# Kernel tuning notes

Measured on AMD Instinct MI355X. Metric: run time of the kernel, lower is better.

The kernel has to match this reference:

```python
import jax, jax.numpy as jnp
import numpy as np
import math

C, F, NH, W = 8, 256, 8, 1024  # channels, features (h), num_heads, frames (w)


def conv3x3(x, w):
    # x: [b,c,h,w], w: [out_c,in_c,3,3], padding=1, stride=1, no bias
    return jax.lax.conv_general_dilated(
        x, w, window_strides=(1, 1), padding=((1, 1), (1, 1)),
        dimension_numbers=("NCHW", "OIHW", "NCHW"))


def mc_linear_pw(x, w_pw):
    # per-channel linear over the feature (h) axis
    # x: [b,c,h,w], w_pw: [c, h_out, h_in] -> [b,c,h_out,w]
    return jnp.einsum("bchw,cgh->bcgw", x, w_pw)


def setup_inputs() -> dict:
    key = jax.random.key(0)
    ks = jax.random.split(key, 11)
    conv_s = 1.0 / math.sqrt(C * 9)
    pw_s = 1.0 / math.sqrt(F)
    dw_s = 1.0 / math.sqrt(C)
    return {
        "x": jax.random.normal(ks[0], (1, C, F, W), jnp.float32),
        "prev_qk": jax.random.normal(ks[1], (1, C, NH, W, W), jnp.float32),
        "wq_conv": jax.random.normal(ks[2], (C, C, 3, 3), jnp.float32) * conv_s,
        "wk_conv": jax.random.normal(ks[3], (C, C, 3, 3), jnp.float32) * conv_s,
        "wv_conv": jax.random.normal(ks[4], (C, C, 3, 3), jnp.float32) * conv_s,
        "wq_pw": jax.random.normal(ks[5], (C, F, F), jnp.float32) * pw_s,
        "wk_pw": jax.random.normal(ks[6], (C, F, F), jnp.float32) * pw_s,
        "wv_pw": jax.random.normal(ks[7], (C, F, F), jnp.float32) * pw_s,
        "wo_dw": jax.random.normal(ks[8], (C, C), jnp.float32) * dw_s,
        "wo_pw": jax.random.normal(ks[9], (C, F, F), jnp.float32) * pw_s,
    }


def reference(x, prev_qk, wq_conv, wk_conv, wv_conv, wq_pw, wk_pw, wv_pw, wo_dw, wo_pw):
    b, c, h, w = x.shape
    dh = h // NH

    def proj_heads(inp, w_conv, w_pw):
        p = mc_linear_pw(conv3x3(inp, w_conv), w_pw)          # [b,c,h,w]
        p = jnp.transpose(p, (0, 1, 3, 2))                     # [b,c,w,h]
        p = p.reshape(b, c, w, NH, dh)                         # [b,c,w,nh,dh]
        return jnp.transpose(p, (0, 1, 3, 2, 4))               # [b,c,nh,w,dh]

    q = proj_heads(x, wq_conv, wq_pw)
    k = proj_heads(x, wk_conv, wk_pw)
    v = proj_heads(x, wv_conv, wv_pw)

    # attention in fp32 over the frame (w) axis, scaled by sqrt(h) (features)
    qk = jnp.einsum("bcnqd,bcnkd->bcnqk", q.astype(jnp.float32), k.astype(jnp.float32)) / math.sqrt(h)
    qk = qk + prev_qk
    a = jnp.einsum("bcnqk,bcnkd->bcnqd", jax.nn.softmax(qk, axis=-1), v.astype(jnp.float32))
    a = jnp.transpose(a, (0, 1, 3, 2, 4)).reshape(b, c, w, h)  # [b,c,w,h]
    a = jnp.transpose(a, (0, 1, 3, 2))                          # [b,c,h,w]

    # o_proj: depthwise channel mix then per-channel positionwise linear
    o = jnp.einsum("bchw,dc->bdhw", a, wo_dw)
    out = mc_linear_pw(o, wo_pw)
    return (out, qk)
```

## Files before the change

kernel.cpp:

```cpp
#include <hip/hip_runtime.h>
#include <hip/hip_bf16.h>


typedef float f32x4 __attribute__((ext_vector_type(4)));
typedef short s16x8 __attribute__((ext_vector_type(8)));

static __device__ __forceinline__ unsigned short f2bf(float f) {
  unsigned int u = __builtin_bit_cast(unsigned int, f);
  u += 0x7fff + ((u >> 16) & 1);
  return (unsigned short)(u >> 16);
}

__global__ __launch_bounds__(256) void cvt_weights(
    const float* __restrict__ wq, const float* __restrict__ wk,
    const float* __restrict__ wv, const float* __restrict__ wo,
    unsigned short* __restrict__ dst) {
  int gid = blockIdx.x * 256 + threadIdx.x;
  int e = gid * 4;
  int arr = e >> 19;
  int off = e & 524287;
  const float* src = arr == 0 ? wq : arr == 1 ? wk : arr == 2 ? wv : wo;
  float4 v = *(const float4*)(src + off);
  ushort4 o;
  o.x = f2bf(v.x); o.y = f2bf(v.y); o.z = f2bf(v.z); o.w = f2bf(v.w);
  *(ushort4*)(dst + (size_t)arr * 524288 + off) = o;
}

__global__ __launch_bounds__(256) void conv3x3_k(
    const float* __restrict__ x,
    const float* __restrict__ wq, const float* __restrict__ wk,
    const float* __restrict__ wv,
    unsigned short* __restrict__ convT) {
  __shared__ float xt[8][34][36];
  int t = blockIdx.z;
  const float* wc = (t == 0) ? wq : (t == 1) ? wk : wv;
  int wtile = blockIdx.x * 32, htile = blockIdx.y * 32;
  int tid = threadIdx.x;
  for (int i = tid; i < 8 * 34 * 34; i += 256) {
    int cp = i / 1156;
    int rem = i - cp * 1156;
    int hh = rem / 34, ww = rem - hh * 34;
    int gh = htile + hh - 1, gw = wtile + ww - 1;
    float v = 0.f;
    if ((unsigned)gh < 256u && (unsigned)gw < 1024u)
      v = x[((size_t)cp * 256 + gh) * 1024 + gw];
    xt[cp][hh][ww] = v;
  }
  __syncthreads();
  int tx = tid & 31, strip = tid >> 5;
  int h0 = strip * 4;
  float acc[8][4];
#pragma unroll
  for (int co = 0; co < 8; ++co)
#pragma unroll
    for (int p = 0; p < 4; ++p) acc[co][p] = 0.f;
#pragma unroll 1
  for (int cp = 0; cp < 8; ++cp) {
    float xv[6][3];
#pragma unroll
    for (int rr = 0; rr < 6; ++rr)
#pragma unroll
      for (int cc = 0; cc < 3; ++cc)
        xv[rr][cc] = xt[cp][h0 + rr][tx + cc];
#pragma unroll
    for (int i = 0; i < 3; ++i)
#pragma unroll
      for (int j = 0; j < 3; ++j) {
#pragma unroll
        for (int co = 0; co < 8; ++co) {
          float wgt = wc[((co * 8 + cp) * 3 + i) * 3 + j];
#pragma unroll
          for (int p = 0; p < 4; ++p)
            acc[co][p] += wgt * xv[p + i][j];
        }
      }
  }
  int w = wtile + tx;
#pragma unroll
  for (int co = 0; co < 8; ++co) {
    ushort4 o;
    o.x = f2bf(acc[co][0]); o.y = f2bf(acc[co][1]);
    o.z = f2bf(acc[co][2]); o.w = f2bf(acc[co][3]);
    *(ushort4*)(convT + ((size_t)(t * 8 + co) * 1024 + w) * 256 + htile + h0) = o;
  }
}

__global__ __launch_bounds__(256) void gemm_pw(
    const unsigned short* __restrict__ A0,
    const unsigned short* __restrict__ B0,
    unsigned short* __restrict__ qkh,
    unsigned short* __restrict__ vstd,
    float* __restrict__ outp,
    int mode) {
  int b = blockIdx.z;
  const unsigned short* A = A0 + (size_t)b * 65536;
  const unsigned short* B = B0 + (size_t)b * 262144;
  int lane = threadIdx.x & 63, wvid = threadIdx.x >> 6;
  int wm = wvid & 1, wn = wvid >> 1;
  int mBase = blockIdx.y * 128 + wm * 64;
  int nBase = blockIdx.x * 128 + wn * 64;
  int c15 = lane & 15, klo = (lane >> 4) * 8;
  f32x4 acc[4][4];
#pragma unroll
  for (int mi = 0; mi < 4; ++mi)
#pragma unroll
    for (int ni = 0; ni < 4; ++ni) acc[mi][ni] = (f32x4){0.f, 0.f, 0.f, 0.f};
#pragma unroll 2
  for (int kk = 0; kk < 256; kk += 32) {
    s16x8 af[4], bf[4];
#pragma unroll
    for (int mi = 0; mi < 4; ++mi)
      af[mi] = *(const s16x8*)(A + (size_t)(mBase + mi * 16 + c15) * 256 + kk + klo);
#pragma unroll
    for (int ni = 0; ni < 4; ++ni)
      bf[ni] = *(const s16x8*)(B + (size_t)(nBase + ni * 16 + c15) * 256 + kk + klo);
#pragma unroll
    for (int mi = 0; mi < 4; ++mi)
#pragma unroll
      for (int ni = 0; ni < 4; ++ni)
        acc[mi][ni] = __builtin_amdgcn_mfma_f32_16x16x32_bf16(
            af[mi], bf[ni], acc[mi][ni], 0, 0, 0);
  }
  int r0 = (lane >> 4) * 4;
  if (mode == 0) {
    int t = b >> 3, c = b & 7;
    if (t < 2) {
      unsigned short* dst = qkh + (size_t)t * 2097152 + (size_t)c * 262144;
#pragma unroll
      for (int mi = 0; mi < 4; ++mi)
#pragma unroll
        for (int ni = 0; ni < 4; ++ni) {
          int g = mBase + mi * 16 + r0;
          int w = nBase + ni * 16 + c15;
          int n = g >> 5, d = g & 31;
          ushort4 o;
          o.x = f2bf(acc[mi][ni][0]); o.y = f2bf(acc[mi][ni][1]);
          o.z = f2bf(acc[mi][ni][2]); o.w = f2bf(acc[mi][ni][3]);
          *(ushort4*)(dst + ((size_t)n * 1024 + w) * 32 + d) = o;
        }
    } else {
      unsigned short* dst = vstd + (size_t)c * 262144;
#pragma unroll
      for (int mi = 0; mi < 4; ++mi)
#pragma unroll
        for (int ni = 0; ni < 4; ++ni) {
          int w = nBase + ni * 16 + c15;
#pragma unroll
          for (int r = 0; r < 4; ++r)
            dst[(size_t)(mBase + mi * 16 + r0 + r) * 1024 + w] = f2bf(acc[mi][ni][r]);
        }
    }
  } else {
    float* dst = outp + (size_t)b * 262144;
#pragma unroll
    for (int mi = 0; mi < 4; ++mi)
#pragma unroll
      for (int ni = 0; ni < 4; ++ni) {
        int w = nBase + ni * 16 + c15;
#pragma unroll
        for (int r = 0; r < 4; ++r)
          dst[(size_t)(mBase + mi * 16 + r0 + r) * 1024 + w] = acc[mi][ni][r];
      }
  }
}

__global__ __launch_bounds__(256) void attn_k(
    const unsigned short* __restrict__ Qh,
    const unsigned short* __restrict__ Kh,
    const unsigned short* __restrict__ Vstd,
    const float* __restrict__ prev,
    float* __restrict__ qkOut,
    float* __restrict__ aOut) {
  __shared__ unsigned short plds[4][16 * 72];
  int lane = threadIdx.x & 63, wvid = threadIdx.x >> 6;
  int cn = blockIdx.y;
  int c = cn >> 3, n = cn & 7;
  int qBase = blockIdx.x * 64 + wvid * 16;
  int c15 = lane & 15, quad = lane >> 4, klo = quad * 8;
  const unsigned short* Q = Qh + (size_t)cn * 32768;
  const unsigned short* K = Kh + (size_t)cn * 32768;
  const unsigned short* V = Vstd + (size_t)c * 262144 + (size_t)n * 32 * 1024;
  const float* prevB = prev + (size_t)cn * 1048576 + (size_t)(qBase + c15) * 1024 + quad * 4;
  float* qkB = qkOut + (size_t)cn * 1048576 + (size_t)(qBase + c15) * 1024 + quad * 4;
  s16x8 qf = *(const s16x8*)(Q + (size_t)(qBase + c15) * 32 + klo);
  f32x4 o0 = {0.f, 0.f, 0.f, 0.f}, o1 = {0.f, 0.f, 0.f, 0.f};
  float lsum = 0.f;
  unsigned short* pw = plds[wvid];

  f32x4 pvA[4];
  s16x8 kfA[4];
#pragma unroll
  for (int kt = 0; kt < 4; ++kt) {
    kfA[kt] = *(const s16x8*)(K + (size_t)(kt * 16 + c15) * 32 + klo);
    pvA[kt] = *(const f32x4*)(prevB + kt * 16);
  }

#pragma unroll 1
  for (int kb = 0; kb < 1024; kb += 64) {
    int kbn = (kb + 64) & 1023;
    f32x4 s2[4];
#pragma unroll
    for (int kt = 0; kt < 4; ++kt) {
      f32x4 z = {0.f, 0.f, 0.f, 0.f};
      s2[kt] = __builtin_amdgcn_mfma_f32_16x16x32_bf16(kfA[kt], qf, z, 0, 0, 0);
    }
    s16x8 vf[2][2];
#pragma unroll
    for (int kk2 = 0; kk2 < 2; ++kk2) {
      vf[kk2][0] = *(const s16x8*)(V + (size_t)c15 * 1024 + kb + kk2 * 32 + klo);
      vf[kk2][1] = *(const s16x8*)(V + (size_t)(16 + c15) * 1024 + kb + kk2 * 32 + klo);
    }
    f32x4 pvN[4];
    s16x8 kfN[4];
#pragma unroll
    for (int kt = 0; kt < 4; ++kt) {
      kfN[kt] = *(const s16x8*)(K + (size_t)(kbn + kt * 16 + c15) * 32 + klo);
      pvN[kt] = *(const f32x4*)(prevB + kbn + kt * 16);
    }
#pragma unroll
    for (int kt = 0; kt < 4; ++kt) {
      f32x4 val = s2[kt] * 0.0625f + pvA[kt];
      *(f32x4*)(qkB + kb + kt * 16) = val;
      float p0 = __expf(val[0]), p1 = __expf(val[1]),
            p2 = __expf(val[2]), p3 = __expf(val[3]);
      lsum += (p0 + p1) + (p2 + p3);
      ushort4 pk;
      pk.x = f2bf(p0); pk.y = f2bf(p1); pk.z = f2bf(p2); pk.w = f2bf(p3);
      *(ushort4*)(pw + c15 * 72 + kt * 16 + quad * 4) = pk;
    }
#pragma unroll
    for (int kk2 = 0; kk2 < 2; ++kk2) {
      s16x8 pf = *(const s16x8*)(pw + c15 * 72 + kk2 * 32 + klo);
      o0 = __builtin_amdgcn_mfma_f32_16x16x32_bf16(pf, vf[kk2][0], o0, 0, 0, 0);
      o1 = __builtin_amdgcn_mfma_f32_16x16x32_bf16(pf, vf[kk2][1], o1, 0, 0, 0);
    }
#pragma unroll
    for (int kt = 0; kt < 4; ++kt) {
      kfA[kt] = kfN[kt];
      pvA[kt] = pvN[kt];
    }
  }
  lsum += __shfl_xor(lsum, 16);
  lsum += __shfl_xor(lsum, 32);
#pragma unroll
  for (int r = 0; r < 4; ++r) {
    float inv = 1.0f / __shfl(lsum, quad * 4 + r);
    int q = qBase + quad * 4 + r;
    aOut[((size_t)c * 256 + n * 32 + c15) * 1024 + q] = o0[r] * inv;
    aOut[((size_t)c * 256 + n * 32 + 16 + c15) * 1024 + q] = o1[r] * inv;
  }
}

__global__ __launch_bounds__(256) void mix_t(
    const float* __restrict__ a, const float* __restrict__ dw,
    unsigned short* __restrict__ ot) {
  int tx = threadIdx.x & 31, strip = threadIdx.x >> 5;
  int wtile = blockIdx.x * 32, htile = blockIdx.y * 32;
  int w = wtile + tx, h0 = htile + strip * 4;
  float acc[8][4];
#pragma unroll
  for (int co = 0; co < 8; ++co)
#pragma unroll
    for (int p = 0; p < 4; ++p) acc[co][p] = 0.f;
#pragma unroll 1
  for (int cp = 0; cp < 8; ++cp) {
    float av[4];
#pragma unroll
    for (int p = 0; p < 4; ++p)
      av[p] = a[((size_t)cp * 256 + h0 + p) * 1024 + w];
#pragma unroll
    for (int co = 0; co < 8; ++co) {
      float wgt = dw[co * 8 + cp];
#pragma unroll
      for (int p = 0; p < 4; ++p) acc[co][p] += wgt * av[p];
    }
  }
#pragma unroll
  for (int co = 0; co < 8; ++co) {
    ushort4 o;
    o.x = f2bf(acc[co][0]); o.y = f2bf(acc[co][1]);
    o.z = f2bf(acc[co][2]); o.w = f2bf(acc[co][3]);
    *(ushort4*)(ot + ((size_t)co * 1024 + w) * 256 + h0) = o;
  }
}

extern "C" void kernel_launch(void* const* d_in, const int* in_sizes, int n_in,
                              void* d_out, int out_size, void* d_ws, size_t ws_size,
                              hipStream_t stream) {
  (void)in_sizes; (void)n_in; (void)out_size; (void)ws_size;
  const float* x       = (const float*)d_in[0];
  const float* prev    = (const float*)d_in[1];
  const float* wq_conv = (const float*)d_in[2];
  const float* wk_conv = (const float*)d_in[3];
  const float* wv_conv = (const float*)d_in[4];
  const float* wq_pw   = (const float*)d_in[5];
  const float* wk_pw   = (const float*)d_in[6];
  const float* wv_pw   = (const float*)d_in[7];
  const float* wo_dw   = (const float*)d_in[8];
  const float* wo_pw   = (const float*)d_in[9];

  float* outp  = (float*)d_out;
  float* qkOut = outp + 2097152;

  char* ws = (char*)d_ws;
  unsigned short* pwB   = (unsigned short*)ws;
  unsigned short* convT = (unsigned short*)(ws + (4  << 20));
  unsigned short* qkh   = (unsigned short*)(ws + (16 << 20));
  unsigned short* vstd  = (unsigned short*)(ws + (24 << 20));
  float*          aBuf  = (float*)         (ws + (28 << 20));
  unsigned short* otB   = (unsigned short*)(ws + (36 << 20));

  cvt_weights<<<2048, 256, 0, stream>>>(wq_pw, wk_pw, wv_pw, wo_pw, pwB);
  conv3x3_k<<<dim3(32, 8, 3), 256, 0, stream>>>(x, wq_conv, wk_conv, wv_conv, convT);
  gemm_pw<<<dim3(8, 2, 24), 256, 0, stream>>>(pwB, convT, qkh, vstd, nullptr, 0);
  attn_k<<<dim3(16, 64), 256, 0, stream>>>(qkh, qkh + 2097152, vstd, prev, qkOut, aBuf);
  mix_t<<<dim3(32, 8), 256, 0, stream>>>(aBuf, wo_dw, otB);
  gemm_pw<<<dim3(8, 2, 8), 256, 0, stream>>>(pwB + 3 * 524288, otB, nullptr, nullptr, outp, 1);
}
```

Measured before the change: 581.8 us.

## Transpose QK scores through LDS for row-contiguous prev/qk access in attention

```diff
diff --git a/kernel.cpp b/kernel.cpp
--- a/kernel.cpp
+++ b/kernel.cpp
@@ -164,13 +164,14 @@
   }
 }
 
-__global__ __launch_bounds__(256) void attn_k(
+__global__ __launch_bounds__(256, 4) void attn_k(
     const unsigned short* __restrict__ Qh,
     const unsigned short* __restrict__ Kh,
     const unsigned short* __restrict__ Vstd,
     const float* __restrict__ prev,
     float* __restrict__ qkOut,
     float* __restrict__ aOut) {
+  __shared__ float slds[4][16 * 68 + 16];
   __shared__ unsigned short plds[4][16 * 72];
   int lane = threadIdx.x & 63, wvid = threadIdx.x >> 6;
   int cn = blockIdx.y;
@@ -179,21 +180,19 @@
   int c15 = lane & 15, quad = lane >> 4, klo = quad * 8;
   const unsigned short* Q = Qh + (size_t)cn * 32768;
   const unsigned short* K = Kh + (size_t)cn * 32768;
-  const unsigned short* V = Vstd + (size_t)c * 262144 + (size_t)n * 32 * 1024;
-  const float* prevB = prev + (size_t)cn * 1048576 + (size_t)(qBase + c15) * 1024 + quad * 4;
-  float* qkB = qkOut + (size_t)cn * 1048576 + (size_t)(qBase + c15) * 1024 + quad * 4;
+  const unsigned short* V = Vstd + (size_t)c * 262144 + (size_t)n * 32768;
+  float* sw = slds[wvid];
+  unsigned short* pw = plds[wvid];
+  const float* prevR = prev + (size_t)cn * 1048576 + (size_t)(qBase + quad) * 1024 + c15 * 4;
+  float* qkR = qkOut + (size_t)cn * 1048576 + (size_t)(qBase + quad) * 1024 + c15 * 4;
   s16x8 qf = *(const s16x8*)(Q + (size_t)(qBase + c15) * 32 + klo);
   f32x4 o0 = {0.f, 0.f, 0.f, 0.f}, o1 = {0.f, 0.f, 0.f, 0.f};
-  float lsum = 0.f;
-  unsigned short* pw = plds[wvid];
+  float lsum[4] = {0.f, 0.f, 0.f, 0.f};
 
   f32x4 pvA[4];
-  s16x8 kfA[4];
-#pragma unroll
-  for (int kt = 0; kt < 4; ++kt) {
-    kfA[kt] = *(const s16x8*)(K + (size_t)(kt * 16 + c15) * 32 + klo);
-    pvA[kt] = *(const f32x4*)(prevB + kt * 16);
-  }
+#pragma unroll
+  for (int j = 0; j < 4; ++j)
+    pvA[j] = *(const f32x4*)(prevR + (size_t)j * 4096);
 
 #pragma unroll 1
   for (int kb = 0; kb < 1024; kb += 64) {
@@ -201,32 +200,40 @@
     f32x4 s2[4];
 #pragma unroll
     for (int kt = 0; kt < 4; ++kt) {
+      s16x8 kf = *(const s16x8*)(K + (size_t)(kb + kt * 16 + c15) * 32 + klo);
       f32x4 z = {0.f, 0.f, 0.f, 0.f};
-      s2[kt] = __builtin_amdgcn_mfma_f32_16x16x32_bf16(kfA[kt], qf, z, 0, 0, 0);
-    }
+      s2[kt] = __builtin_amdgcn_mfma_f32_16x16x32_bf16(kf, qf, z, 0, 0, 0);
+    }
+    f32x4 pvN[4];
+#pragma unroll
+    for (int j = 0; j < 4; ++j)
+      pvN[j] = *(const f32x4*)(prevR + (size_t)j * 4096 + kbn);
     s16x8 vf[2][2];
 #pragma unroll
     for (int kk2 = 0; kk2 < 2; ++kk2) {
       vf[kk2][0] = *(const s16x8*)(V + (size_t)c15 * 1024 + kb + kk2 * 32 + klo);
       vf[kk2][1] = *(const s16x8*)(V + (size_t)(16 + c15) * 1024 + kb + kk2 * 32 + klo);
     }
-    f32x4 pvN[4];
-    s16x8 kfN[4];
-#pragma unroll
-    for (int kt = 0; kt < 4; ++kt) {
-      kfN[kt] = *(const s16x8*)(K + (size_t)(kbn + kt * 16 + c15) * 32 + klo);
-      pvN[kt] = *(const f32x4*)(prevB + kbn + kt * 16);
-    }
-#pragma unroll
-    for (int kt = 0; kt < 4; ++kt) {
-      f32x4 val = s2[kt] * 0.0625f + pvA[kt];
-      *(f32x4*)(qkB + kb + kt * 16) = val;
-      float p0 = __expf(val[0]), p1 = __expf(val[1]),
-            p2 = __expf(val[2]), p3 = __expf(val[3]);
-      lsum += (p0 + p1) + (p2 + p3);
+#pragma unroll
+    for (int kt = 0; kt < 4; ++kt)
+      *(f32x4*)(sw + c15 * 68 + kt * 16 + quad * 4) = s2[kt];
+    f32x4 val[4];
+#pragma unroll
+    for (int j = 0; j < 4; ++j)
+      val[j] = *(const f32x4*)(sw + (4 * j + quad) * 68 + c15 * 4);
+#pragma unroll
+    for (int j = 0; j < 4; ++j) {
+      val[j] = val[j] * 0.0625f + pvA[j];
+      __builtin_nontemporal_store(val[j], (f32x4*)(qkR + (size_t)j * 4096 + kb));
+    }
+#pragma unroll
+    for (int j = 0; j < 4; ++j) {
+      float p0 = __expf(val[j][0]), p1 = __expf(val[j][1]),
+            p2 = __expf(val[j][2]), p3 = __expf(val[j][3]);
+      lsum[j] += (p0 + p1) + (p2 + p3);
       ushort4 pk;
       pk.x = f2bf(p0); pk.y = f2bf(p1); pk.z = f2bf(p2); pk.w = f2bf(p3);
-      *(ushort4*)(pw + c15 * 72 + kt * 16 + quad * 4) = pk;
+      *(ushort4*)(pw + (4 * j + quad) * 72 + c15 * 4) = pk;
     }
 #pragma unroll
     for (int kk2 = 0; kk2 < 2; ++kk2) {
@@ -235,16 +242,18 @@
       o1 = __builtin_amdgcn_mfma_f32_16x16x32_bf16(pf, vf[kk2][1], o1, 0, 0, 0);
     }
 #pragma unroll
-    for (int kt = 0; kt < 4; ++kt) {
-      kfA[kt] = kfN[kt];
-      pvA[kt] = pvN[kt];
-    }
-  }
-  lsum += __shfl_xor(lsum, 16);
-  lsum += __shfl_xor(lsum, 32);
+    for (int j = 0; j < 4; ++j) pvA[j] = pvN[j];
+  }
+#pragma unroll
+  for (int j = 0; j < 4; ++j) {
+    float s = lsum[j];
+    s += __shfl_xor(s, 1); s += __shfl_xor(s, 2);
+    s += __shfl_xor(s, 4); s += __shfl_xor(s, 8);
+    if (c15 == 0) sw[16 * 68 + 4 * j + quad] = s;
+  }
 #pragma unroll
   for (int r = 0; r < 4; ++r) {
-    float inv = 1.0f / __shfl(lsum, quad * 4 + r);
+    float inv = 1.0f / sw[16 * 68 + quad * 4 + r];
     int q = qBase + quad * 4 + r;
     aOut[((size_t)c * 256 + n * 32 + c15) * 1024 + q] = o0[r] * inv;
     aOut[((size_t)c * 256 + n * 32 + 16 + c15) * 1024 + q] = o1[r] * inv;
```

Result: no change. 579.2 us (-0.5%).

## Restage attention scores through swizzled LDS for coalesced row-wise qk/prev access

Applied to the files above, without the earlier changes.

```diff
diff --git a/kernel.cpp b/kernel.cpp
--- a/kernel.cpp
+++ b/kernel.cpp
@@ -164,14 +164,14 @@
   }
 }
 
-__global__ __launch_bounds__(256) void attn_k(
+__global__ __launch_bounds__(256, 2) void attn_k(
     const unsigned short* __restrict__ Qh,
     const unsigned short* __restrict__ Kh,
     const unsigned short* __restrict__ Vstd,
     const float* __restrict__ prev,
     float* __restrict__ qkOut,
     float* __restrict__ aOut) {
-  __shared__ unsigned short plds[4][16 * 72];
+  __shared__ char ldsRaw[4][16384];
   int lane = threadIdx.x & 63, wvid = threadIdx.x >> 6;
   int cn = blockIdx.y;
   int c = cn >> 3, n = cn & 7;
@@ -179,75 +179,65 @@
   int c15 = lane & 15, quad = lane >> 4, klo = quad * 8;
   const unsigned short* Q = Qh + (size_t)cn * 32768;
   const unsigned short* K = Kh + (size_t)cn * 32768;
-  const unsigned short* V = Vstd + (size_t)c * 262144 + (size_t)n * 32 * 1024;
-  const float* prevB = prev + (size_t)cn * 1048576 + (size_t)(qBase + c15) * 1024 + quad * 4;
-  float* qkB = qkOut + (size_t)cn * 1048576 + (size_t)(qBase + c15) * 1024 + quad * 4;
+  const unsigned short* V = Vstd + (size_t)c * 262144 + (size_t)n * 32768;
+  char* base = ldsRaw[wvid];
+  const float* prevB = prev + (size_t)cn * 1048576;
+  float* qkB = qkOut + (size_t)cn * 1048576;
   s16x8 qf = *(const s16x8*)(Q + (size_t)(qBase + c15) * 32 + klo);
   f32x4 o0 = {0.f, 0.f, 0.f, 0.f}, o1 = {0.f, 0.f, 0.f, 0.f};
-  float lsum = 0.f;
-  unsigned short* pw = plds[wvid];
-
-  f32x4 pvA[4];
-  s16x8 kfA[4];
-#pragma unroll
-  for (int kt = 0; kt < 4; ++kt) {
-    kfA[kt] = *(const s16x8*)(K + (size_t)(kt * 16 + c15) * 32 + klo);
-    pvA[kt] = *(const f32x4*)(prevB + kt * 16);
-  }
+  float lsum[16];
+#pragma unroll
+  for (int r = 0; r < 16; ++r) lsum[r] = 0.f;
 
 #pragma unroll 1
-  for (int kb = 0; kb < 1024; kb += 64) {
-    int kbn = (kb + 64) & 1023;
-    f32x4 s2[4];
-#pragma unroll
-    for (int kt = 0; kt < 4; ++kt) {
+  for (int kb = 0; kb < 1024; kb += 256) {
+#pragma unroll
+    for (int kt = 0; kt < 16; ++kt) {
+      s16x8 kf = *(const s16x8*)(K + (size_t)(kb + kt * 16 + c15) * 32 + klo);
       f32x4 z = {0.f, 0.f, 0.f, 0.f};
-      s2[kt] = __builtin_amdgcn_mfma_f32_16x16x32_bf16(kfA[kt], qf, z, 0, 0, 0);
-    }
-    s16x8 vf[2][2];
-#pragma unroll
-    for (int kk2 = 0; kk2 < 2; ++kk2) {
-      vf[kk2][0] = *(const s16x8*)(V + (size_t)c15 * 1024 + kb + kk2 * 32 + klo);
-      vf[kk2][1] = *(const s16x8*)(V + (size_t)(16 + c15) * 1024 + kb + kk2 * 32 + klo);
-    }
-    f32x4 pvN[4];
-    s16x8 kfN[4];
-#pragma unroll
-    for (int kt = 0; kt < 4; ++kt) {
-      kfN[kt] = *(const s16x8*)(K + (size_t)(kbn + kt * 16 + c15) * 32 + klo);
-      pvN[kt] = *(const f32x4*)(prevB + kbn + kt * 16);
-    }
-#pragma unroll
-    for (int kt = 0; kt < 4; ++kt) {
-      f32x4 val = s2[kt] * 0.0625f + pvA[kt];
-      *(f32x4*)(qkB + kb + kt * 16) = val;
+      f32x4 s2 = __builtin_amdgcn_mfma_f32_16x16x32_bf16(kf, qf, z, 0, 0, 0);
+      *(f32x4*)(base + c15 * 1024 + (((kt * 4 + quad) ^ (c15 & 7)) << 4)) = s2;
+    }
+#pragma unroll
+    for (int r = 0; r < 16; ++r) {
+      f32x4 sv = *(const f32x4*)(base + r * 1024 + ((lane ^ (r & 7)) << 4));
+      f32x4 pv = *(const f32x4*)(prevB + (size_t)(qBase + r) * 1024 + kb + lane * 4);
+      f32x4 val = sv * 0.0625f + pv;
+      __builtin_nontemporal_store(val,
+          (f32x4*)(qkB + (size_t)(qBase + r) * 1024 + kb + lane * 4));
       float p0 = __expf(val[0]), p1 = __expf(val[1]),
             p2 = __expf(val[2]), p3 = __expf(val[3]);
-      lsum += (p0 + p1) + (p2 + p3);
+      lsum[r] += (p0 + p1) + (p2 + p3);
       ushort4 pk;
       pk.x = f2bf(p0); pk.y = f2bf(p1); pk.z = f2bf(p2); pk.w = f2bf(p3);
-      *(ushort4*)(pw + c15 * 72 + kt * 16 + quad * 4) = pk;
-    }
-#pragma unroll
-    for (int kk2 = 0; kk2 < 2; ++kk2) {
-      s16x8 pf = *(const s16x8*)(pw + c15 * 72 + kk2 * 32 + klo);
-      o0 = __builtin_amdgcn_mfma_f32_16x16x32_bf16(pf, vf[kk2][0], o0, 0, 0, 0);
-      o1 = __builtin_amdgcn_mfma_f32_16x16x32_bf16(pf, vf[kk2][1], o1, 0, 0, 0);
-    }
-#pragma unroll
-    for (int kt = 0; kt < 4; ++kt) {
-      kfA[kt] = kfN[kt];
-      pvA[kt] = pvN[kt];
-    }
-  }
-  lsum += __shfl_xor(lsum, 16);
-  lsum += __shfl_xor(lsum, 32);
-#pragma unroll
-  for (int r = 0; r < 4; ++r) {
-    float inv = 1.0f / __shfl(lsum, quad * 4 + r);
-    int q = qBase + quad * 4 + r;
-    aOut[((size_t)c * 256 + n * 32 + c15) * 1024 + q] = o0[r] * inv;
-    aOut[((size_t)c * 256 + n * 32 + 16 + c15) * 1024 + q] = o1[r] * inv;
+      *(ushort4*)(base + r * 1024 + 512 +
+                  ((((lane >> 1) ^ (r & 7)) << 4) | ((lane & 1) << 3))) = pk;
+    }
+#pragma unroll
+    for (int kk2 = 0; kk2 < 8; ++kk2) {
+      s16x8 pf = *(const s16x8*)(base + c15 * 1024 + 512 +
+                                 ((((kk2 * 4 + quad) ^ (c15 & 7)) << 4)));
+      s16x8 v0 = *(const s16x8*)(V + (size_t)c15 * 1024 + kb + kk2 * 32 + klo);
+      s16x8 v1 = *(const s16x8*)(V + (size_t)(16 + c15) * 1024 + kb + kk2 * 32 + klo);
+      o0 = __builtin_amdgcn_mfma_f32_16x16x32_bf16(pf, v0, o0, 0, 0, 0);
+      o1 = __builtin_amdgcn_mfma_f32_16x16x32_bf16(pf, v1, o1, 0, 0, 0);
+    }
+  }
+  float* swf = (float*)base;
+#pragma unroll
+  for (int r = 0; r < 16; ++r) {
+    float t = lsum[r];
+    t += __shfl_xor(t, 1);  t += __shfl_xor(t, 2);
+    t += __shfl_xor(t, 4);  t += __shfl_xor(t, 8);
+    t += __shfl_xor(t, 16); t += __shfl_xor(t, 32);
+    if (lane == 0) swf[r] = t;
+  }
+#pragma unroll
+  for (int rr = 0; rr < 4; ++rr) {
+    float inv = 1.0f / swf[quad * 4 + rr];
+    int q = qBase + quad * 4 + rr;
+    aOut[((size_t)c * 256 + n * 32 + c15) * 1024 + q] = o0[rr] * inv;
+    aOut[((size_t)c * 256 + n * 32 + 16 + c15) * 1024 + q] = o1[rr] * inv;
   }
 }
 
```

Result: slower. 646.3 us (+11.1%).

## Split attention key range across two blocks with atomic partial-sum combine

Applied to the files above, without the earlier changes.

```diff
diff --git a/kernel.cpp b/kernel.cpp
--- a/kernel.cpp
+++ b/kernel.cpp
@@ -164,22 +164,29 @@
   }
 }
 
-__global__ __launch_bounds__(256) void attn_k(
+__global__ __launch_bounds__(256) void zero_ws(float4* __restrict__ dst) {
+  dst[(size_t)blockIdx.x * 256 + threadIdx.x] =
+      make_float4(0.f, 0.f, 0.f, 0.f);
+}
+
+__global__ __launch_bounds__(256, 8) void attn_k(
     const unsigned short* __restrict__ Qh,
     const unsigned short* __restrict__ Kh,
     const unsigned short* __restrict__ Vstd,
     const float* __restrict__ prev,
     float* __restrict__ qkOut,
-    float* __restrict__ aOut) {
+    float* __restrict__ Opart,
+    float* __restrict__ lpart) {
   __shared__ unsigned short plds[4][16 * 72];
   int lane = threadIdx.x & 63, wvid = threadIdx.x >> 6;
   int cn = blockIdx.y;
   int c = cn >> 3, n = cn & 7;
   int qBase = blockIdx.x * 64 + wvid * 16;
+  int kb0 = blockIdx.z << 9;
   int c15 = lane & 15, quad = lane >> 4, klo = quad * 8;
   const unsigned short* Q = Qh + (size_t)cn * 32768;
   const unsigned short* K = Kh + (size_t)cn * 32768;
-  const unsigned short* V = Vstd + (size_t)c * 262144 + (size_t)n * 32 * 1024;
+  const unsigned short* V = Vstd + (size_t)c * 262144 + (size_t)n * 32768;
   const float* prevB = prev + (size_t)cn * 1048576 + (size_t)(qBase + c15) * 1024 + quad * 4;
   float* qkB = qkOut + (size_t)cn * 1048576 + (size_t)(qBase + c15) * 1024 + quad * 4;
   s16x8 qf = *(const s16x8*)(Q + (size_t)(qBase + c15) * 32 + klo);
@@ -191,13 +198,14 @@
   s16x8 kfA[4];
 #pragma unroll
   for (int kt = 0; kt < 4; ++kt) {
-    kfA[kt] = *(const s16x8*)(K + (size_t)(kt * 16 + c15) * 32 + klo);
-    pvA[kt] = *(const f32x4*)(prevB + kt * 16);
+    kfA[kt] = *(const s16x8*)(K + (size_t)(kb0 + kt * 16 + c15) * 32 + klo);
+    pvA[kt] = *(const f32x4*)(prevB + kb0 + kt * 16);
   }
 
 #pragma unroll 1
-  for (int kb = 0; kb < 1024; kb += 64) {
-    int kbn = (kb + 64) & 1023;
+  for (int ko = 0; ko < 512; ko += 64) {
+    int kb = kb0 + ko;
+    int kbn = kb0 + ((ko + 64) & 511);
     f32x4 s2[4];
 #pragma unroll
     for (int kt = 0; kt < 4; ++kt) {
@@ -242,12 +250,30 @@
   }
   lsum += __shfl_xor(lsum, 16);
   lsum += __shfl_xor(lsum, 32);
+  float* OpartB = Opart + (size_t)cn * 32768;
+  if (quad == 0) atomicAdd(lpart + cn * 1024 + qBase + c15, lsum);
 #pragma unroll
   for (int r = 0; r < 4; ++r) {
-    float inv = 1.0f / __shfl(lsum, quad * 4 + r);
     int q = qBase + quad * 4 + r;
-    aOut[((size_t)c * 256 + n * 32 + c15) * 1024 + q] = o0[r] * inv;
-    aOut[((size_t)c * 256 + n * 32 + 16 + c15) * 1024 + q] = o1[r] * inv;
+    atomicAdd(OpartB + (size_t)c15 * 1024 + q, o0[r]);
+    atomicAdd(OpartB + (size_t)(16 + c15) * 1024 + q, o1[r]);
+  }
+}
+
+__global__ __launch_bounds__(256) void combine_k(
+    const float* __restrict__ Opart, const float* __restrict__ lpart,
+    float* __restrict__ aOut) {
+  int cn = blockIdx.y;
+  int c = cn >> 3, n = cn & 7;
+  int lane = threadIdx.x & 63;
+  int q = blockIdx.x * 64 + lane;
+  int dg = threadIdx.x >> 6;
+  float inv = 1.0f / lpart[cn * 1024 + q];
+#pragma unroll
+  for (int dd = 0; dd < 8; ++dd) {
+    int d = dg * 8 + dd;
+    aOut[((size_t)(c * 256) + n * 32 + d) * 1024 + q] =
+        Opart[((size_t)cn * 32 + d) * 1024 + q] * inv;
   }
 }
 
@@ -305,6 +331,8 @@
   char* ws = (char*)d_ws;
   unsigned short* pwB   = (unsigned short*)ws;
   unsigned short* convT = (unsigned short*)(ws + (4  << 20));
+  float*          Opart = (float*)         (ws + (4  << 20));
+  float*          lpart = (float*)         (ws + (12 << 20));
   unsigned short* qkh   = (unsigned short*)(ws + (16 << 20));
   unsigned short* vstd  = (unsigned short*)(ws + (24 << 20));
   float*          aBuf  = (float*)         (ws + (28 << 20));
@@ -313,7 +341,10 @@
   cvt_weights<<<2048, 256, 0, stream>>>(wq_pw, wk_pw, wv_pw, wo_pw, pwB);
   conv3x3_k<<<dim3(32, 8, 3), 256, 0, stream>>>(x, wq_conv, wk_conv, wv_conv, convT);
   gemm_pw<<<dim3(8, 2, 24), 256, 0, stream>>>(pwB, convT, qkh, vstd, nullptr, 0);
-  attn_k<<<dim3(16, 64), 256, 0, stream>>>(qkh, qkh + 2097152, vstd, prev, qkOut, aBuf);
+  zero_ws<<<2112, 256, 0, stream>>>((float4*)Opart);
+  attn_k<<<dim3(16, 64, 2), 256, 0, stream>>>(qkh, qkh + 2097152, vstd, prev,
+                                              qkOut, Opart, lpart);
+  combine_k<<<dim3(16, 64), 256, 0, stream>>>(Opart, lpart, aBuf);
   mix_t<<<dim3(32, 8), 256, 0, stream>>>(aBuf, wo_dw, otB);
   gemm_pw<<<dim3(8, 2, 8), 256, 0, stream>>>(pwB + 3 * 524288, otB, nullptr, nullptr, outp, 1);
 }
```

Measured after the change: 645.7 us. 11.0% more time.
